# Kernel optimization log

Hardware: AMD Instinct MI355X
Metric: run time of the kernel (lower is better)

## Reference

```python
import jax, jax.numpy as jnp
import numpy as np

DIMS = 1024
VOCAB = 32000
BATCH = 128
SEQ = 512


def setup_inputs() -> dict:
    key = jax.random.key(0)
    ks = jax.random.split(key, 10)
    s = 1.0 / np.sqrt(DIMS)
    inp = {
        'features': jax.random.randint(ks[0], (BATCH, SEQ), 0, VOCAB, dtype=jnp.int32),
        'embeddings': jax.random.normal(ks[1], (VOCAB, DIMS), dtype=jnp.float32) * s,
        'Wf': jax.random.normal(ks[2], (DIMS, DIMS), dtype=jnp.float32) * s,
        'Uf': jax.random.normal(ks[3], (DIMS, DIMS), dtype=jnp.float32) * s,
        'bf': jnp.zeros((1, DIMS), dtype=jnp.float32),
        'Wi': jax.random.normal(ks[4], (DIMS, DIMS), dtype=jnp.float32) * s,
        'Ui': jax.random.normal(ks[5], (DIMS, DIMS), dtype=jnp.float32) * s,
        'bi': jnp.zeros((1, DIMS), dtype=jnp.float32),
        'Wo': jax.random.normal(ks[6], (DIMS, DIMS), dtype=jnp.float32) * s,
        'Uo': jax.random.normal(ks[7], (DIMS, DIMS), dtype=jnp.float32) * s,
        'bo': jnp.zeros((1, DIMS), dtype=jnp.float32),
        'Wc': jax.random.normal(ks[8], (DIMS, DIMS), dtype=jnp.float32) * s,
        'Uc': jax.random.normal(ks[9], (DIMS, DIMS), dtype=jnp.float32) * s,
        'bc': jnp.zeros((1, DIMS), dtype=jnp.float32),
    }
    return inp


def reference(features, embeddings, Wf, Uf, bf, Wi, Ui, bi, Wo, Uo, bo, Wc, Uc, bc):
    # Embedding lookup for all timesteps: (B, T, D) -> (T, B, D) for scan
    x = embeddings[features]  # (B, T, D)
    x = jnp.transpose(x, (1, 0, 2))  # (T, B, D)
    B = features.shape[0]
    h0 = jnp.zeros((B, DIMS), dtype=embeddings.dtype)
    c0 = jnp.zeros((B, DIMS), dtype=embeddings.dtype)

    def step(carry, xt):
        h, c = carry
        ft = jax.nn.sigmoid(xt @ Wf + h @ Uf + bf)
        ot = jax.nn.sigmoid(xt @ Wo + h @ Uo + bo)
        it = jax.nn.sigmoid(xt @ Wi + h @ Ui + bi)
        ct = jnp.tanh(xt @ Wc + h @ Uc + bc)
        c = ft * c + it * ct
        h = ot * jnp.tanh(c)
        return (h, c), None

    (h, c), _ = jax.lax.scan(step, (h0, c0), x)
    return jnp.concatenate([h, c], axis=1)  # (B, 2*D)
```

## Files before the change

### kernel.cpp

```cpp
#include <hip/hip_runtime.h>
#include <hip/hip_bf16.h>

#define DIMS 1024
#define SEQ 512
#define BATCH 128
#define VOCAB 32000
#define GRID 256

typedef __attribute__((ext_vector_type(8))) short short8;
typedef __attribute__((ext_vector_type(4))) float f32x4;

__device__ __forceinline__ ushort f2bf(float x) {
    union { float f; unsigned u; } v; v.f = x;
    unsigned u = v.u;
    return (ushort)((u + 0x7FFFu + ((u >> 16) & 1u)) >> 16);
}

__global__ void conv_emb_kernel(const float* __restrict__ in, ushort* __restrict__ out, int n) {
    int idx = blockIdx.x * blockDim.x + threadIdx.x;
    int stride = gridDim.x * blockDim.x;
    for (int i = idx * 4; i < n; i += stride * 4) {
        float4 v = *(const float4*)(in + i);
        ushort4 o;
        o.x = f2bf(v.x); o.y = f2bf(v.y); o.z = f2bf(v.z); o.w = f2bf(v.w);
        *(ushort4*)(out + i) = o;
    }
}

__launch_bounds__(512, 2)
__global__ void lstm_kernel(const int* __restrict__ feats,
                            const ushort* __restrict__ emb,
                            const float* __restrict__ Wf, const float* __restrict__ Uf, const float* __restrict__ bfp,
                            const float* __restrict__ Wi, const float* __restrict__ Ui, const float* __restrict__ bip,
                            const float* __restrict__ Wo, const float* __restrict__ Uo, const float* __restrict__ bop,
                            const float* __restrict__ Wc, const float* __restrict__ Uc, const float* __restrict__ bcp,
                            ushort* __restrict__ hbuf, float* __restrict__ out, int* __restrict__ flags) {
    __shared__ ushort Bl[32 * 2048];
    __shared__ float pre0[64 * 36];
    __shared__ float pre1[64 * 36];

    const int tid = threadIdx.x;
    const int bid = blockIdx.x;
    const int rg = bid >> 7;
    const int cb = bid & 127;

    for (int idx = tid; idx < 32 * 2048; idx += 512) {
        int cl = idx & 31;
        int k  = idx >> 5;
        int g  = cl >> 3, dd0 = cl & 7;
        int dw = cb * 8 + dd0;
        const float* Wg = (g == 0) ? Wf : (g == 1) ? Wi : (g == 2) ? Wo : Wc;
        const float* Ug = (g == 0) ? Uf : (g == 1) ? Ui : (g == 2) ? Uo : Uc;
        float v = (k < 1024) ? Wg[k * 1024 + dw] : Ug[(k - 1024) * 1024 + dw];
        int boff = ((cl << 12) | (k << 1)) ^ ((cl & 7) << 4);
        *(ushort*)((char*)Bl + boff) = f2bf(v);
    }

    const int lane = tid & 63;
    const int w  = tid >> 6;
    const int wr = w & 3;
    const int kh = w >> 2;
    const int lx = lane & 15;
    const int qq = lane >> 4;
    const int kg = qq * 8;
    const int lr = wr * 16 + lx;
    const int brow = rg * 64 + lr;

    const int bofs0 = (lx << 12) ^ ((lx & 7) << 4);
    const int bofs1 = ((16 + lx) << 12) ^ ((lx & 7) << 4);

    const int kb    = kh * 512;
    const int fbase = kh * 64;
    float* myPre = kh ? pre1 : pre0;
    const int r0 = wr * 16 + qq * 4;

    const int grow_ = tid >> 3;
    const int gdd   = tid & 7;
    const int gd    = cb * 8 + gdd;
    const float bF = bfp[gd], bI = bip[gd], bO = bop[gd], bC = bcp[gd];

    float cst = 0.f;
    int* myflags = flags + rg * 128;
    int fidx = feats[brow * SEQ];

    __syncthreads();

    for (int t = 0; t < SEQ; t++) {
        f32x4 a00 = {0,0,0,0}, a01 = {0,0,0,0};
        f32x4 a10 = {0,0,0,0}, a11 = {0,0,0,0};

        const ushort* xrow = emb + (size_t)fidx * DIMS;
        fidx = (t + 1 < SEQ) ? feats[brow * SEQ + t + 1] : 0;

        #pragma unroll
        for (int ks = 0; ks < 8; ks += 2) {
            {
                int k = kb + ks * 32 + kg;
                short8 a  = *(const short8*)(xrow + k);
                short8 b0 = *(const short8*)((const char*)Bl + (bofs0 ^ (k << 1)));
                short8 b1 = *(const short8*)((const char*)Bl + (bofs1 ^ (k << 1)));
                a00 = __builtin_amdgcn_mfma_f32_16x16x32_bf16(a, b0, a00, 0, 0, 0);
                a10 = __builtin_amdgcn_mfma_f32_16x16x32_bf16(a, b1, a10, 0, 0, 0);
            }
            {
                int k = kb + (ks + 1) * 32 + kg;
                short8 a  = *(const short8*)(xrow + k);
                short8 b0 = *(const short8*)((const char*)Bl + (bofs0 ^ (k << 1)));
                short8 b1 = *(const short8*)((const char*)Bl + (bofs1 ^ (k << 1)));
                a01 = __builtin_amdgcn_mfma_f32_16x16x32_bf16(a, b0, a01, 0, 0, 0);
                a11 = __builtin_amdgcn_mfma_f32_16x16x32_bf16(a, b1, a11, 0, 0, 0);
            }
        }

        union { unsigned long long u[2]; short8 v; } hv[16];
        if (t > 0) {
            long guard = 0;
            for (;;) {
                int f0 = __hip_atomic_load(myflags + fbase + lane, __ATOMIC_RELAXED, __HIP_MEMORY_SCOPE_AGENT);
                if (__all(f0 >= t)) break;
                __builtin_amdgcn_s_sleep(1);
                if (++guard > 100000000L) break;
            }
            const ushort* hbase = hbuf + (size_t)((t & 1) * 2 + rg) * (128 * 512);
            #pragma unroll
            for (int ks = 0; ks < 16; ks++) {
                int chunk = fbase + ks * 4 + qq;
                const unsigned long long* hp =
                    (const unsigned long long*)(hbase + (chunk << 9) + lr * 8);
                hv[ks].u[0] = __hip_atomic_load(hp,     __ATOMIC_RELAXED, __HIP_MEMORY_SCOPE_AGENT);
                hv[ks].u[1] = __hip_atomic_load(hp + 1, __ATOMIC_RELAXED, __HIP_MEMORY_SCOPE_AGENT);
            }
        }

        #pragma unroll
        for (int ks = 8; ks < 16; ks += 2) {
            {
                int k = kb + ks * 32 + kg;
                short8 a  = *(const short8*)(xrow + k);
                short8 b0 = *(const short8*)((const char*)Bl + (bofs0 ^ (k << 1)));
                short8 b1 = *(const short8*)((const char*)Bl + (bofs1 ^ (k << 1)));
                a00 = __builtin_amdgcn_mfma_f32_16x16x32_bf16(a, b0, a00, 0, 0, 0);
                a10 = __builtin_amdgcn_mfma_f32_16x16x32_bf16(a, b1, a10, 0, 0, 0);
            }
            {
                int k = kb + (ks + 1) * 32 + kg;
                short8 a  = *(const short8*)(xrow + k);
                short8 b0 = *(const short8*)((const char*)Bl + (bofs0 ^ (k << 1)));
                short8 b1 = *(const short8*)((const char*)Bl + (bofs1 ^ (k << 1)));
                a01 = __builtin_amdgcn_mfma_f32_16x16x32_bf16(a, b0, a01, 0, 0, 0);
                a11 = __builtin_amdgcn_mfma_f32_16x16x32_bf16(a, b1, a11, 0, 0, 0);
            }
        }

        if (t > 0) {
            #pragma unroll
            for (int ks = 0; ks < 16; ks += 2) {
                {
                    int k = 1024 + kb + ks * 32 + kg;
                    short8 b0 = *(const short8*)((const char*)Bl + (bofs0 ^ (k << 1)));
                    short8 b1 = *(const short8*)((const char*)Bl + (bofs1 ^ (k << 1)));
                    a00 = __builtin_amdgcn_mfma_f32_16x16x32_bf16(hv[ks].v, b0, a00, 0, 0, 0);
                    a10 = __builtin_amdgcn_mfma_f32_16x16x32_bf16(hv[ks].v, b1, a10, 0, 0, 0);
                }
                {
                    int k = 1024 + kb + (ks + 1) * 32 + kg;
                    short8 b0 = *(const short8*)((const char*)Bl + (bofs0 ^ (k << 1)));
                    short8 b1 = *(const short8*)((const char*)Bl + (bofs1 ^ (k << 1)));
                    a01 = __builtin_amdgcn_mfma_f32_16x16x32_bf16(hv[ks + 1].v, b0, a01, 0, 0, 0);
                    a11 = __builtin_amdgcn_mfma_f32_16x16x32_bf16(hv[ks + 1].v, b1, a11, 0, 0, 0);
                }
            }
        }

        #pragma unroll
        for (int j = 0; j < 4; j++) {
            myPre[(r0 + j) * 36 + lx]      = a00[j] + a01[j];
            myPre[(r0 + j) * 36 + 16 + lx] = a10[j] + a11[j];
        }
        __syncthreads();

        {
            int base = grow_ * 36;
            float pf = pre0[base + gdd]      + pre1[base + gdd]      + bF;
            float pi = pre0[base + 8 + gdd]  + pre1[base + 8 + gdd]  + bI;
            float po = pre0[base + 16 + gdd] + pre1[base + 16 + gdd] + bO;
            float pc = pre0[base + 24 + gdd] + pre1[base + 24 + gdd] + bC;
            float f  = 1.f / (1.f + __expf(-pf));
            float ig = 1.f / (1.f + __expf(-pi));
            float o  = 1.f / (1.f + __expf(-po));
            float e2 = __expf(2.f * pc);
            float cc = (e2 - 1.f) / (e2 + 1.f);
            float cn = f * cst + ig * cc;
            cst = cn;
            float e2c = __expf(2.f * cn);
            float th  = (e2c - 1.f) / (e2c + 1.f);
            float h   = o * th;
            if (t < SEQ - 1) {
                ushort* hw = hbuf + (size_t)(((t + 1) & 1) * 2 + rg) * (128 * 512) + cb * 512 + tid;
                __hip_atomic_store(hw, f2bf(h), __ATOMIC_RELAXED, __HIP_MEMORY_SCOPE_AGENT);
            } else {
                int gr = rg * 64 + grow_;
                out[gr * 2048 + gd] = h;
                out[gr * 2048 + 1024 + gd] = cn;
            }
        }

        if (t < SEQ - 1) {
            asm volatile("s_waitcnt vmcnt(0)" ::: "memory");
            __syncthreads();
            if (tid == 0) {
                __hip_atomic_store(myflags + cb, t + 1, __ATOMIC_RELAXED, __HIP_MEMORY_SCOPE_AGENT);
            }
        }
    }
}

extern "C" void kernel_launch(void* const* d_in, const int* in_sizes, int n_in,
                              void* d_out, int out_size, void* d_ws, size_t ws_size,
                              hipStream_t stream) {
    const int*   feats = (const int*)d_in[0];
    const float* emb_f = (const float*)d_in[1];
    const float* Wf = (const float*)d_in[2];
    const float* Uf = (const float*)d_in[3];
    const float* bf_ = (const float*)d_in[4];
    const float* Wi = (const float*)d_in[5];
    const float* Ui = (const float*)d_in[6];
    const float* bi_ = (const float*)d_in[7];
    const float* Wo = (const float*)d_in[8];
    const float* Uo = (const float*)d_in[9];
    const float* bo_ = (const float*)d_in[10];
    const float* Wc = (const float*)d_in[11];
    const float* Uc = (const float*)d_in[12];
    const float* bc_ = (const float*)d_in[13];

    char* ws = (char*)d_ws;
    ushort* emb_bf = (ushort*)ws;
    ushort* hbuf   = (ushort*)(ws + 65536000);
    int*    flags  = (int*)(ws + 65536000 + 524288);

    hipMemsetAsync(flags, 0, 1024, stream);
    conv_emb_kernel<<<1024, 256, 0, stream>>>(emb_f, emb_bf, VOCAB * DIMS);
    lstm_kernel<<<GRID, 512, 0, stream>>>(feats, emb_bf,
                                          Wf, Uf, bf_, Wi, Ui, bi_,
                                          Wo, Uo, bo_, Wc, Uc, bc_,
                                          hbuf, (float*)d_out, flags);
}
```

Before: 4.161 ms.

## Replicate hidden state per XCD and drop separate embedding conversion kernel

Each block reads its XCC_ID, takes a rank within that XCD, and copies one 1KB slice of the previous h into a per-XCD replica buffer. It then signals a per-XCD flag, and all consumers read h from the local replica with sc0 loads, which avoids cross-die L2 traffic on the recurrent critical path. The bf16 conversion of the embedding table is removed. Embedding rows are now read as fp32 and packed to bf16 inline, which doubles per-step gather bytes but skips converting the full 32000x1024 table. The change adds an extra two-level synchronization per step and assumes exactly 32 blocks land on each XCD.

```diff
diff --git a/kernel.cpp b/kernel.cpp
--- a/kernel.cpp
+++ b/kernel.cpp
@@ -16,28 +16,29 @@
     return (ushort)((u + 0x7FFFu + ((u >> 16) & 1u)) >> 16);
 }
 
-__global__ void conv_emb_kernel(const float* __restrict__ in, ushort* __restrict__ out, int n) {
-    int idx = blockIdx.x * blockDim.x + threadIdx.x;
-    int stride = gridDim.x * blockDim.x;
-    for (int i = idx * 4; i < n; i += stride * 4) {
-        float4 v = *(const float4*)(in + i);
-        ushort4 o;
-        o.x = f2bf(v.x); o.y = f2bf(v.y); o.z = f2bf(v.z); o.w = f2bf(v.w);
-        *(ushort4*)(out + i) = o;
-    }
-}
-
-__launch_bounds__(512, 2)
+__device__ __forceinline__ short8 pack8(const float* p) {
+    float4 f0 = *(const float4*)p;
+    float4 f1 = *(const float4*)(p + 4);
+    union { ushort us[8]; short8 v; } r;
+    r.us[0] = f2bf(f0.x); r.us[1] = f2bf(f0.y); r.us[2] = f2bf(f0.z); r.us[3] = f2bf(f0.w);
+    r.us[4] = f2bf(f1.x); r.us[5] = f2bf(f1.y); r.us[6] = f2bf(f1.z); r.us[7] = f2bf(f1.w);
+    return r.v;
+}
+
+__launch_bounds__(512, 1)
 __global__ void lstm_kernel(const int* __restrict__ feats,
-                            const ushort* __restrict__ emb,
+                            const float* __restrict__ emb,
                             const float* __restrict__ Wf, const float* __restrict__ Uf, const float* __restrict__ bfp,
                             const float* __restrict__ Wi, const float* __restrict__ Ui, const float* __restrict__ bip,
                             const float* __restrict__ Wo, const float* __restrict__ Uo, const float* __restrict__ bop,
                             const float* __restrict__ Wc, const float* __restrict__ Uc, const float* __restrict__ bcp,
-                            ushort* __restrict__ hbuf, float* __restrict__ out, int* __restrict__ flags) {
+                            ushort* __restrict__ hbuf, float* __restrict__ out,
+                            int* __restrict__ flags, int* __restrict__ xcdcnt,
+                            int* __restrict__ xcdfl, ushort* __restrict__ xcdbuf) {
     __shared__ ushort Bl[32 * 2048];
     __shared__ float pre0[64 * 36];
     __shared__ float pre1[64 * 36];
+    __shared__ int s_xcd, s_rank;
 
     const int tid = threadIdx.x;
     const int bid = blockIdx.x;
@@ -56,6 +57,17 @@
         *(ushort*)((char*)Bl + boff) = f2bf(v);
     }
 
+    if (tid == 0) {
+        int x;
+        asm("s_getreg_b32 %0, hwreg(HW_REG_XCC_ID)" : "=s"(x));
+        x &= 7;
+        s_xcd = x;
+        s_rank = atomicAdd(&xcdcnt[x], 1) & 31;
+    }
+    __syncthreads();
+    const int xcd = s_xcd;
+    const int rank = s_rank;
+
     const int lane = tid & 63;
     const int w  = tid >> 6;
     const int wr = w & 3;
@@ -74,29 +86,29 @@
     float* myPre = kh ? pre1 : pre0;
     const int r0 = wr * 16 + qq * 4;
 
+    const int gcw = rank * 8 + w;
+
     const int grow_ = tid >> 3;
     const int gdd   = tid & 7;
     const int gd    = cb * 8 + gdd;
     const float bF = bfp[gd], bI = bip[gd], bO = bop[gd], bC = bcp[gd];
 
     float cst = 0.f;
-    int* myflags = flags + rg * 128;
     int fidx = feats[brow * SEQ];
-
-    __syncthreads();
 
     for (int t = 0; t < SEQ; t++) {
         f32x4 a00 = {0,0,0,0}, a01 = {0,0,0,0};
         f32x4 a10 = {0,0,0,0}, a11 = {0,0,0,0};
 
-        const ushort* xrow = emb + (size_t)fidx * DIMS;
+        const float* xrow = emb + (size_t)fidx * DIMS;
         fidx = (t + 1 < SEQ) ? feats[brow * SEQ + t + 1] : 0;
+        const int par = t & 1;
 
         #pragma unroll
         for (int ks = 0; ks < 8; ks += 2) {
             {
                 int k = kb + ks * 32 + kg;
-                short8 a  = *(const short8*)(xrow + k);
+                short8 a  = pack8(xrow + k);
                 short8 b0 = *(const short8*)((const char*)Bl + (bofs0 ^ (k << 1)));
                 short8 b1 = *(const short8*)((const char*)Bl + (bofs1 ^ (k << 1)));
                 a00 = __builtin_amdgcn_mfma_f32_16x16x32_bf16(a, b0, a00, 0, 0, 0);
@@ -104,7 +116,7 @@
             }
             {
                 int k = kb + (ks + 1) * 32 + kg;
-                short8 a  = *(const short8*)(xrow + k);
+                short8 a  = pack8(xrow + k);
                 short8 b0 = *(const short8*)((const char*)Bl + (bofs0 ^ (k << 1)));
                 short8 b1 = *(const short8*)((const char*)Bl + (bofs1 ^ (k << 1)));
                 a01 = __builtin_amdgcn_mfma_f32_16x16x32_bf16(a, b0, a01, 0, 0, 0);
@@ -112,62 +124,85 @@
             }
         }
 
-        union { unsigned long long u[2]; short8 v; } hv[16];
         if (t > 0) {
             long guard = 0;
-            for (;;) {
-                int f0 = __hip_atomic_load(myflags + fbase + lane, __ATOMIC_RELAXED, __HIP_MEMORY_SCOPE_AGENT);
-                if (__all(f0 >= t)) break;
+            while (__hip_atomic_load(&flags[gcw], __ATOMIC_RELAXED, __HIP_MEMORY_SCOPE_AGENT) < t) {
                 __builtin_amdgcn_s_sleep(1);
                 if (++guard > 100000000L) break;
             }
-            const ushort* hbase = hbuf + (size_t)((t & 1) * 2 + rg) * (128 * 512);
+            const unsigned long long* rp = (const unsigned long long*)
+                (hbuf + ((size_t)par * 256 + gcw) * 512 + lane * 8);
+            union { unsigned long long u[2]; short8 v; } rv;
+            rv.u[0] = __hip_atomic_load(rp,     __ATOMIC_RELAXED, __HIP_MEMORY_SCOPE_AGENT);
+            rv.u[1] = __hip_atomic_load(rp + 1, __ATOMIC_RELAXED, __HIP_MEMORY_SCOPE_AGENT);
+            short8* wp = (short8*)
+                (xcdbuf + (((size_t)xcd * 2 + par) * 256 + gcw) * 512 + lane * 8);
+            *wp = rv.v;
+            asm volatile("s_waitcnt vmcnt(0)" ::: "memory");
+            __syncthreads();
+            if (tid == 0) {
+                __hip_atomic_store(&xcdfl[xcd * 32 + rank], t,
+                                   __ATOMIC_RELAXED, __HIP_MEMORY_SCOPE_AGENT);
+            }
+        }
+
+        #pragma unroll
+        for (int ks = 8; ks < 16; ks += 2) {
+            {
+                int k = kb + ks * 32 + kg;
+                short8 a  = pack8(xrow + k);
+                short8 b0 = *(const short8*)((const char*)Bl + (bofs0 ^ (k << 1)));
+                short8 b1 = *(const short8*)((const char*)Bl + (bofs1 ^ (k << 1)));
+                a00 = __builtin_amdgcn_mfma_f32_16x16x32_bf16(a, b0, a00, 0, 0, 0);
+                a10 = __builtin_amdgcn_mfma_f32_16x16x32_bf16(a, b1, a10, 0, 0, 0);
+            }
+            {
+                int k = kb + (ks + 1) * 32 + kg;
+                short8 a  = pack8(xrow + k);
+                short8 b0 = *(const short8*)((const char*)Bl + (bofs0 ^ (k << 1)));
+                short8 b1 = *(const short8*)((const char*)Bl + (bofs1 ^ (k << 1)));
+                a01 = __builtin_amdgcn_mfma_f32_16x16x32_bf16(a, b0, a01, 0, 0, 0);
+                a11 = __builtin_amdgcn_mfma_f32_16x16x32_bf16(a, b1, a11, 0, 0, 0);
+            }
+        }
+
+        if (t > 0) {
+            {
+                long guard = 0;
+                for (;;) {
+                    int v = __hip_atomic_load(&xcdfl[xcd * 32 + (lane & 31)],
+                                              __ATOMIC_RELAXED, __HIP_MEMORY_SCOPE_AGENT);
+                    if (__all(v >= t)) break;
+                    __builtin_amdgcn_s_sleep(1);
+                    if (++guard > 100000000L) break;
+                }
+            }
+            const ushort* xb = xcdbuf + ((size_t)xcd * 2 + par) * (256 * 512)
+                                      + (size_t)rg * (128 * 512);
+            short8 hv[16];
             #pragma unroll
             for (int ks = 0; ks < 16; ks++) {
-                int chunk = fbase + ks * 4 + qq;
-                const unsigned long long* hp =
-                    (const unsigned long long*)(hbase + (chunk << 9) + lr * 8);
-                hv[ks].u[0] = __hip_atomic_load(hp,     __ATOMIC_RELAXED, __HIP_MEMORY_SCOPE_AGENT);
-                hv[ks].u[1] = __hip_atomic_load(hp + 1, __ATOMIC_RELAXED, __HIP_MEMORY_SCOPE_AGENT);
-            }
-        }
-
-        #pragma unroll
-        for (int ks = 8; ks < 16; ks += 2) {
-            {
-                int k = kb + ks * 32 + kg;
-                short8 a  = *(const short8*)(xrow + k);
-                short8 b0 = *(const short8*)((const char*)Bl + (bofs0 ^ (k << 1)));
-                short8 b1 = *(const short8*)((const char*)Bl + (bofs1 ^ (k << 1)));
-                a00 = __builtin_amdgcn_mfma_f32_16x16x32_bf16(a, b0, a00, 0, 0, 0);
-                a10 = __builtin_amdgcn_mfma_f32_16x16x32_bf16(a, b1, a10, 0, 0, 0);
-            }
-            {
-                int k = kb + (ks + 1) * 32 + kg;
-                short8 a  = *(const short8*)(xrow + k);
-                short8 b0 = *(const short8*)((const char*)Bl + (bofs0 ^ (k << 1)));
-                short8 b1 = *(const short8*)((const char*)Bl + (bofs1 ^ (k << 1)));
-                a01 = __builtin_amdgcn_mfma_f32_16x16x32_bf16(a, b0, a01, 0, 0, 0);
-                a11 = __builtin_amdgcn_mfma_f32_16x16x32_bf16(a, b1, a11, 0, 0, 0);
-            }
-        }
-
-        if (t > 0) {
+                const ushort* hp = xb + ((fbase + ks * 4 + qq) << 9) + lr * 8;
+                asm volatile("global_load_dwordx4 %0, %1, off sc0"
+                             : "=v"(hv[ks]) : "v"(hp));
+            }
+            asm volatile("s_waitcnt vmcnt(0)" ::: "memory");
+            __builtin_amdgcn_sched_barrier(0);
             #pragma unroll
             for (int ks = 0; ks < 16; ks += 2) {
                 {
                     int k = 1024 + kb + ks * 32 + kg;
                     short8 b0 = *(const short8*)((const char*)Bl + (bofs0 ^ (k << 1)));
                     short8 b1 = *(const short8*)((const char*)Bl + (bofs1 ^ (k << 1)));
-                    a00 = __builtin_amdgcn_mfma_f32_16x16x32_bf16(hv[ks].v, b0, a00, 0, 0, 0);
-                    a10 = __builtin_amdgcn_mfma_f32_16x16x32_bf16(hv[ks].v, b1, a10, 0, 0, 0);
+                    a00 = __builtin_amdgcn_mfma_f32_16x16x32_bf16(hv[ks], b0, a00, 0, 0, 0);
+                    a10 = __builtin_amdgcn_mfma_f32_16x16x32_bf16(hv[ks], b1, a10, 0, 0, 0);
                 }
                 {
                     int k = 1024 + kb + (ks + 1) * 32 + kg;
                     short8 b0 = *(const short8*)((const char*)Bl + (bofs0 ^ (k << 1)));
                     short8 b1 = *(const short8*)((const char*)Bl + (bofs1 ^ (k << 1)));
-                    a01 = __builtin_amdgcn_mfma_f32_16x16x32_bf16(hv[ks + 1].v, b0, a01, 0, 0, 0);
-                    a11 = __builtin_amdgcn_mfma_f32_16x16x32_bf16(hv[ks + 1].v, b1, a11, 0, 0, 0);
+                    a01 = __builtin_amdgcn_mfma_f32_16x16x32_bf16(hv[ks + 1], b0, a01, 0, 0, 0);
+                    a11 = __builtin_amdgcn_mfma_f32_16x16x32_bf16(hv[ks + 1], b1, a11, 0, 0, 0);
                 }
             }
         }
@@ -196,7 +231,7 @@
             float th  = (e2c - 1.f) / (e2c + 1.f);
             float h   = o * th;
             if (t < SEQ - 1) {
-                ushort* hw = hbuf + (size_t)(((t + 1) & 1) * 2 + rg) * (128 * 512) + cb * 512 + tid;
+                ushort* hw = hbuf + ((size_t)((t + 1) & 1) * 256 + bid) * 512 + tid;
                 __hip_atomic_store(hw, f2bf(h), __ATOMIC_RELAXED, __HIP_MEMORY_SCOPE_AGENT);
             } else {
                 int gr = rg * 64 + grow_;
@@ -209,7 +244,7 @@
             asm volatile("s_waitcnt vmcnt(0)" ::: "memory");
             __syncthreads();
             if (tid == 0) {
-                __hip_atomic_store(myflags + cb, t + 1, __ATOMIC_RELAXED, __HIP_MEMORY_SCOPE_AGENT);
+                __hip_atomic_store(&flags[bid], t + 1, __ATOMIC_RELAXED, __HIP_MEMORY_SCOPE_AGENT);
             }
         }
     }
@@ -234,14 +269,17 @@
     const float* bc_ = (const float*)d_in[13];
 
     char* ws = (char*)d_ws;
-    ushort* emb_bf = (ushort*)ws;
-    ushort* hbuf   = (ushort*)(ws + 65536000);
-    int*    flags  = (int*)(ws + 65536000 + 524288);
-
-    hipMemsetAsync(flags, 0, 1024, stream);
-    conv_emb_kernel<<<1024, 256, 0, stream>>>(emb_f, emb_bf, VOCAB * DIMS);
-    lstm_kernel<<<GRID, 512, 0, stream>>>(feats, emb_bf,
+    ushort* hbuf   = (ushort*)ws;
+    char*   ctrl   = ws + 524288;
+    int*    flags  = (int*)ctrl;
+    int*    xcdcnt = (int*)(ctrl + 1024);
+    int*    xcdfl  = (int*)(ctrl + 2048);
+    ushort* xcdbuf = (ushort*)(ws + 528384);
+
+    hipMemsetAsync(ctrl, 0, 4096, stream);
+    lstm_kernel<<<GRID, 512, 0, stream>>>(feats, emb_f,
                                           Wf, Uf, bf_, Wi, Ui, bi_,
                                           Wo, Uo, bo_, Wc, Uc, bc_,
-                                          hbuf, (float*)d_out, flags);
-}
+                                          hbuf, (float*)d_out,
+                                          flags, xcdcnt, xcdfl, xcdbuf);
+}
```

Result: slower. 5.823 ms (+40.0%).
